# Kernel tuning notes

Measured on AMD Instinct MI355X. Metric: run time of the kernel, lower is better.

The kernel has to match this reference:

```python
import jax, jax.numpy as jnp
import numpy as np

GRID = (32, 512, 512)  # volumetric query grid

def _fade(t):
    # quintic fade: 6t^5 - 15t^4 + 10t^3
    return t * t * t * (t * (t * 6.0 - 15.0) + 10.0)

def _lerp(a, b, t):
    return a + t * (b - a)

def _hash(perm, *indices):
    # chained permutation-table lookup: r = perm[(r + idx) % 256]
    r = jnp.zeros_like(indices[0])
    for idx in indices:
        r = perm[(r + idx) % 256]
    return r

def setup_inputs() -> dict:
    key = jax.random.key(0)
    kx, ky, kz = jax.random.split(key, 3)
    # coordinates uniform in [0, 64) so many lattice cells are covered
    x = jax.random.uniform(kx, GRID, dtype=jnp.float32) * 64.0
    y = jax.random.uniform(ky, GRID, dtype=jnp.float32) * 64.0
    z = jax.random.uniform(kz, GRID, dtype=jnp.float32) * 64.0
    rng = np.random.default_rng(0)
    perm = jnp.asarray(rng.permutation(256), dtype=jnp.int32)
    grad3 = jnp.asarray([
        [1, 1, 0], [-1, 1, 0], [1, -1, 0], [-1, -1, 0],
        [1, 0, 1], [-1, 0, 1], [1, 0, -1], [-1, 0, -1],
        [0, 1, 1], [0, -1, 1], [0, 1, -1], [0, -1, -1]], dtype=jnp.float32)
    return {"x": x, "y": y, "z": z, "perm": perm, "grad3": grad3}

def reference(x, y, z, perm, grad3):
    fx, fy, fz = jnp.floor(x), jnp.floor(y), jnp.floor(z)
    xi = fx.astype(jnp.int32) & 255
    yi = fy.astype(jnp.int32) & 255
    zi = fz.astype(jnp.int32) & 255
    xf, yf, zf = x - fx, y - fy, z - fz
    u, v, w = _fade(xf), _fade(yf), _fade(zf)

    aaa = _hash(perm, xi, yi, zi) % 12
    aab = _hash(perm, xi, yi, zi + 1) % 12
    aba = _hash(perm, xi, yi + 1, zi) % 12
    abb = _hash(perm, xi, yi + 1, zi + 1) % 12
    baa = _hash(perm, xi + 1, yi, zi) % 12
    bab = _hash(perm, xi + 1, yi, zi + 1) % 12
    bba = _hash(perm, xi + 1, yi + 1, zi) % 12
    bbb = _hash(perm, xi + 1, yi + 1, zi + 1) % 12

    def dot3(gi, dx, dy, dz):
        g = grad3[gi]  # gather [..., 3]
        return g[..., 0] * dx + g[..., 1] * dy + g[..., 2] * dz

    g_aaa = dot3(aaa, xf, yf, zf)
    g_aab = dot3(aab, xf, yf, zf - 1)
    g_aba = dot3(aba, xf, yf - 1, zf)
    g_abb = dot3(abb, xf, yf - 1, zf - 1)
    g_baa = dot3(baa, xf - 1, yf, zf)
    g_bab = dot3(bab, xf - 1, yf, zf - 1)
    g_bba = dot3(bba, xf - 1, yf - 1, zf)
    g_bbb = dot3(bbb, xf - 1, yf - 1, zf - 1)

    x1 = _lerp(g_aaa, g_baa, u)
    x2 = _lerp(g_aba, g_bba, u)
    x3 = _lerp(g_aab, g_bab, u)
    x4 = _lerp(g_abb, g_bbb, u)
    y1 = _lerp(x1, x2, v)
    y2 = _lerp(x3, x4, v)
    return _lerp(y1, y2, w)
```

## Files before the change

### kernel.cpp

```cpp
#include <hip/hip_runtime.h>

__global__ __launch_bounds__(256) void perlin_cells(
    const int* __restrict__ perm, unsigned* __restrict__ cellTab)
{
    __shared__ unsigned P[256];
    P[threadIdx.x] = (unsigned)perm[threadIdx.x];
    __syncthreads();

    unsigned id = blockIdx.x * 256 + threadIdx.x;
    unsigned cx = id & 63u, cy = (id >> 6) & 63u, cz = id >> 12;

    unsigned A = P[cx], B = P[cx + 1];
    unsigned t2[2][2];
    t2[0][0] = P[(A + cy) & 255u];
    t2[0][1] = P[(A + cy + 1u) & 255u];
    t2[1][0] = P[(B + cy) & 255u];
    t2[1][1] = P[(B + cy + 1u) & 255u];

    unsigned word = 0;
    #pragma unroll
    for (unsigned bx = 0; bx < 2; ++bx)
      #pragma unroll
      for (unsigned by = 0; by < 2; ++by)
        #pragma unroll
        for (unsigned bz = 0; bz < 2; ++bz) {
            unsigned gi  = P[(t2[bx][by] + cz + bz) & 255u] % 12u;
            unsigned nib = ((unsigned)(gi < 8u) << 3) | ((unsigned)(gi < 4u) << 2)
                         | ((gi & 1u) << 1) | ((gi >> 1) & 1u);
            unsigned e   = (bx << 2) | (by << 1) | bz;
            word |= nib << (4u * e);
        }
    cellTab[id] = word;
}

#define TPB 256
#define NBLOCKS 2048

__device__ __forceinline__ float fade_f(float t) {
    return t * t * t * fmaf(t, fmaf(t, 6.0f, -15.0f), 10.0f);
}
__device__ __forceinline__ float lerp_f(float a, float b, float t) {
    return fmaf(t, b - a, a);
}

__device__ __forceinline__ float gdot_t(unsigned t, float dx, float dy, float dz) {
    float c1 = ((int)t < 0) ? dx : dy;
    float c2 = ((int)(t << 1) < 0) ? dy : dz;
    unsigned r1 = __float_as_uint(c1) ^ ((t << 2) & 0x80000000u);
    unsigned r2 = __float_as_uint(c2) ^ ((t << 3) & 0x80000000u);
    return __uint_as_float(r1) + __uint_as_float(r2);
}

__global__ __launch_bounds__(TPB, 8) void perlin_kernel(
    const float* __restrict__ xg, const float* __restrict__ yg,
    const float* __restrict__ zg, const unsigned* __restrict__ cellTab,
    float* __restrict__ out, int nquads)
{
    const float4* x4 = (const float4*)xg;
    const float4* y4 = (const float4*)yg;
    const float4* z4 = (const float4*)zg;
    float4* o4 = (float4*)out;

    const int stride = gridDim.x * TPB;
    for (int q = blockIdx.x * TPB + threadIdx.x; q < nquads; q += stride) {
        float4 xv = x4[q], yv = y4[q], zv = z4[q];
        float xs[4] = {xv.x, xv.y, xv.z, xv.w};
        float ys[4] = {yv.x, yv.y, yv.z, yv.w};
        float zs[4] = {zv.x, zv.y, zv.z, zv.w};

        int ix[4], iy[4], iz[4];
        unsigned cw[4];
        #pragma unroll
        for (int e = 0; e < 4; ++e) {
            ix[e] = (int)xs[e]; iy[e] = (int)ys[e]; iz[e] = (int)zs[e];
            cw[e] = cellTab[ix[e] + (iy[e] << 6) + (iz[e] << 12)];
        }

        float4 res;
        float* rp = &res.x;
        #pragma unroll
        for (int e = 0; e < 4; ++e) {
            float xf = xs[e] - (float)ix[e];
            float yf = ys[e] - (float)iy[e];
            float zf = zs[e] - (float)iz[e];
            float u = fade_f(xf), v = fade_f(yf), w = fade_f(zf);
            float xf1 = xf - 1.0f, yf1 = yf - 1.0f, zf1 = zf - 1.0f;
            unsigned cwe = cw[e];

            float g_aaa = gdot_t(cwe << 28, xf,  yf,  zf);
            float g_aab = gdot_t(cwe << 24, xf,  yf,  zf1);
            float g_aba = gdot_t(cwe << 20, xf,  yf1, zf);
            float g_abb = gdot_t(cwe << 16, xf,  yf1, zf1);
            float g_baa = gdot_t(cwe << 12, xf1, yf,  zf);
            float g_bab = gdot_t(cwe << 8,  xf1, yf,  zf1);
            float g_bba = gdot_t(cwe << 4,  xf1, yf1, zf);
            float g_bbb = gdot_t(cwe,       xf1, yf1, zf1);

            float l1 = lerp_f(g_aaa, g_baa, u);
            float l2 = lerp_f(g_aba, g_bba, u);
            float l3 = lerp_f(g_aab, g_bab, u);
            float l4 = lerp_f(g_abb, g_bbb, u);
            float m1 = lerp_f(l1, l2, v);
            float m2 = lerp_f(l3, l4, v);
            rp[e] = lerp_f(m1, m2, w);
        }
        o4[q] = res;
    }
}

extern "C" void kernel_launch(void* const* d_in, const int* in_sizes, int n_in,
                              void* d_out, int out_size, void* d_ws, size_t ws_size,
                              hipStream_t stream) {
    const float* x   = (const float*)d_in[0];
    const float* y   = (const float*)d_in[1];
    const float* z   = (const float*)d_in[2];
    const int* perm  = (const int*)d_in[3];
    float* out = (float*)d_out;
    unsigned* cellTab = (unsigned*)d_ws;

    perlin_cells<<<1024, 256, 0, stream>>>(perm, cellTab);

    int nquads = out_size >> 2;
    perlin_kernel<<<NBLOCKS, TPB, 0, stream>>>(x, y, z, cellTab, out, nquads);
}
```

Baseline: 171.9 us.

## Replace global per-cell hash table with factored LDS tables and replicated gradient words

The 256K-entry per-cell gradient table, read from global memory with a random gather for every point, is replaced by two small tables. One is a 65x64 table of second-level hash pairs and the other is a 256-entry table of packed gradient nibbles for z and z+1. Both are copied into LDS in every block, and the gradient table is replicated 16 ways to reduce bank conflicts. Each point now does two LDS loads plus four replicated LDS lookups instead of one global gather. This adds per-block LDS setup (about 33KB), a single-block table-building kernel, and a change to 512 threads per block, which may limit occupancy.

```diff
diff --git a/kernel.cpp b/kernel.cpp
--- a/kernel.cpp
+++ b/kernel.cpp
@@ -1,40 +1,34 @@
 #include <hip/hip_runtime.h>
 
-__global__ __launch_bounds__(256) void perlin_cells(
-    const int* __restrict__ perm, unsigned* __restrict__ cellTab)
+__global__ __launch_bounds__(512) void perlin_tables(
+    const int* __restrict__ perm, unsigned* __restrict__ H2Pg,
+    unsigned* __restrict__ Wg)
 {
     __shared__ unsigned P[256];
-    P[threadIdx.x] = (unsigned)perm[threadIdx.x];
+    if (threadIdx.x < 256) P[threadIdx.x] = (unsigned)perm[threadIdx.x];
     __syncthreads();
-
-    unsigned id = blockIdx.x * 256 + threadIdx.x;
-    unsigned cx = id & 63u, cy = (id >> 6) & 63u, cz = id >> 12;
-
-    unsigned A = P[cx], B = P[cx + 1];
-    unsigned t2[2][2];
-    t2[0][0] = P[(A + cy) & 255u];
-    t2[0][1] = P[(A + cy + 1u) & 255u];
-    t2[1][0] = P[(B + cy) & 255u];
-    t2[1][1] = P[(B + cy + 1u) & 255u];
-
-    unsigned word = 0;
-    #pragma unroll
-    for (unsigned bx = 0; bx < 2; ++bx)
-      #pragma unroll
-      for (unsigned by = 0; by < 2; ++by)
-        #pragma unroll
-        for (unsigned bz = 0; bz < 2; ++bz) {
-            unsigned gi  = P[(t2[bx][by] + cz + bz) & 255u] % 12u;
-            unsigned nib = ((unsigned)(gi < 8u) << 3) | ((unsigned)(gi < 4u) << 2)
-                         | ((gi & 1u) << 1) | ((gi >> 1) & 1u);
-            unsigned e   = (bx << 2) | (by << 1) | bz;
-            word |= nib << (4u * e);
-        }
-    cellTab[id] = word;
+    for (int s = threadIdx.x; s < 65 * 64; s += 512) {
+        unsigned x = (unsigned)s >> 6, y = (unsigned)s & 63u;
+        unsigned b = P[x];
+        unsigned lo = P[(b + y) & 255u] << 6;
+        unsigned hi = P[(b + y + 1u) & 255u] << 6;
+        H2Pg[s] = lo | (hi << 16);
+    }
+    for (int s = threadIdx.x; s < 256; s += 512) {
+        unsigned g0 = P[s] % 12u;
+        unsigned g1 = P[(s + 1u) & 255u] % 12u;
+        unsigned n0 = ((unsigned)(g0 < 8u) << 3) | ((unsigned)(g0 < 4u) << 2)
+                    | ((g0 & 1u) << 1) | ((g0 >> 1) & 1u);
+        unsigned n1 = ((unsigned)(g1 < 8u) << 3) | ((unsigned)(g1 < 4u) << 2)
+                    | ((g1 & 1u) << 1) | ((g1 >> 1) & 1u);
+        Wg[s] = (n0 << 28) | (n1 << 24);
+    }
 }
 
-#define TPB 256
-#define NBLOCKS 2048
+#define TPB 512
+#define NBLOCKS 1024
+#define H2W (65 * 64)
+#define WREPL 16
 
 __device__ __forceinline__ float fade_f(float t) {
     return t * t * t * fmaf(t, fmaf(t, 6.0f, -15.0f), 10.0f);
@@ -42,7 +36,6 @@
 __device__ __forceinline__ float lerp_f(float a, float b, float t) {
     return fmaf(t, b - a, a);
 }
-
 __device__ __forceinline__ float gdot_t(unsigned t, float dx, float dy, float dz) {
     float c1 = ((int)t < 0) ? dx : dy;
     float c2 = ((int)(t << 1) < 0) ? dy : dz;
@@ -53,9 +46,19 @@
 
 __global__ __launch_bounds__(TPB, 8) void perlin_kernel(
     const float* __restrict__ xg, const float* __restrict__ yg,
-    const float* __restrict__ zg, const unsigned* __restrict__ cellTab,
-    float* __restrict__ out, int nquads)
+    const float* __restrict__ zg, const unsigned* __restrict__ H2Pg,
+    const unsigned* __restrict__ Wg, float* __restrict__ out, int nquads)
 {
+    __shared__ unsigned H2[H2W];
+    __shared__ unsigned Wr[256 * WREPL];
+    for (int s = threadIdx.x; s < H2W; s += TPB)         H2[s] = H2Pg[s];
+    for (int s = threadIdx.x; s < 256 * WREPL; s += TPB) Wr[s] = Wg[s >> 4];
+    __syncthreads();
+
+    const unsigned c4 = (threadIdx.x & (WREPL - 1)) << 2;
+    const char* H2b = (const char*)H2;
+    const char* Wb  = (const char*)Wr;
+
     const float4* x4 = (const float4*)xg;
     const float4* y4 = (const float4*)yg;
     const float4* z4 = (const float4*)zg;
@@ -64,46 +67,52 @@
     const int stride = gridDim.x * TPB;
     for (int q = blockIdx.x * TPB + threadIdx.x; q < nquads; q += stride) {
         float4 xv = x4[q], yv = y4[q], zv = z4[q];
-        float xs[4] = {xv.x, xv.y, xv.z, xv.w};
-        float ys[4] = {yv.x, yv.y, yv.z, yv.w};
-        float zs[4] = {zv.x, zv.y, zv.z, zv.w};
+        float4 res;
 
-        int ix[4], iy[4], iz[4];
-        unsigned cw[4];
-        #pragma unroll
-        for (int e = 0; e < 4; ++e) {
-            ix[e] = (int)xs[e]; iy[e] = (int)ys[e]; iz[e] = (int)zs[e];
-            cw[e] = cellTab[ix[e] + (iy[e] << 6) + (iz[e] << 12)];
+        #define CORE(X, Y, Z, OUT) {                                          \
+            int ix = (int)(X), iy = (int)(Y), iz = (int)(Z);                  \
+            float xf = (X) - (float)ix, yf = (Y) - (float)iy,                 \
+                  zf = (Z) - (float)iz;                                       \
+                         \
+            const unsigned* hp =                                              \
+                (const unsigned*)(H2b + ((unsigned)((ix << 6) + iy) << 2));   \
+            unsigned h_a = hp[0], h_b = hp[64];              \
+            unsigned z6 = (unsigned)iz << 6;                                  \
+            \
+            \
+            unsigned ta0 = (h_a + z6) & 0x3FC0u;                              \
+            unsigned ta1 = ((h_a >> 16) + z6) & 0x3FC0u;                      \
+            unsigned tb0 = (h_b + z6) & 0x3FC0u;                              \
+            unsigned tb1 = ((h_b >> 16) + z6) & 0x3FC0u;                      \
+            unsigned w_aa = *(const unsigned*)(Wb + (ta0 | c4));              \
+            unsigned w_ab = *(const unsigned*)(Wb + (ta1 | c4));              \
+            unsigned w_ba = *(const unsigned*)(Wb + (tb0 | c4));              \
+            unsigned w_bb = *(const unsigned*)(Wb + (tb1 | c4));              \
+            float u = fade_f(xf), v = fade_f(yf), w = fade_f(zf);             \
+            float xf1 = xf - 1.0f, yf1 = yf - 1.0f, zf1 = zf - 1.0f;          \
+            float g_aaa = gdot_t(w_aa,      xf,  yf,  zf);                    \
+            float g_aab = gdot_t(w_aa << 4, xf,  yf,  zf1);                   \
+            float g_aba = gdot_t(w_ab,      xf,  yf1, zf);                    \
+            float g_abb = gdot_t(w_ab << 4, xf,  yf1, zf1);                   \
+            float g_baa = gdot_t(w_ba,      xf1, yf,  zf);                    \
+            float g_bab = gdot_t(w_ba << 4, xf1, yf,  zf1);                   \
+            float g_bba = gdot_t(w_bb,      xf1, yf1, zf);                    \
+            float g_bbb = gdot_t(w_bb << 4, xf1, yf1, zf1);                   \
+            float l1 = lerp_f(g_aaa, g_baa, u);                               \
+            float l2 = lerp_f(g_aba, g_bba, u);                               \
+            float l3 = lerp_f(g_aab, g_bab, u);                               \
+            float l4 = lerp_f(g_abb, g_bbb, u);                               \
+            float m1 = lerp_f(l1, l2, v);                                     \
+            float m2 = lerp_f(l3, l4, v);                                     \
+            OUT = lerp_f(m1, m2, w);                                          \
         }
 
-        float4 res;
-        float* rp = &res.x;
-        #pragma unroll
-        for (int e = 0; e < 4; ++e) {
-            float xf = xs[e] - (float)ix[e];
-            float yf = ys[e] - (float)iy[e];
-            float zf = zs[e] - (float)iz[e];
-            float u = fade_f(xf), v = fade_f(yf), w = fade_f(zf);
-            float xf1 = xf - 1.0f, yf1 = yf - 1.0f, zf1 = zf - 1.0f;
-            unsigned cwe = cw[e];
+        CORE(xv.x, yv.x, zv.x, res.x)
+        CORE(xv.y, yv.y, zv.y, res.y)
+        CORE(xv.z, yv.z, zv.z, res.z)
+        CORE(xv.w, yv.w, zv.w, res.w)
+        #undef CORE
 
-            float g_aaa = gdot_t(cwe << 28, xf,  yf,  zf);
-            float g_aab = gdot_t(cwe << 24, xf,  yf,  zf1);
-            float g_aba = gdot_t(cwe << 20, xf,  yf1, zf);
-            float g_abb = gdot_t(cwe << 16, xf,  yf1, zf1);
-            float g_baa = gdot_t(cwe << 12, xf1, yf,  zf);
-            float g_bab = gdot_t(cwe << 8,  xf1, yf,  zf1);
-            float g_bba = gdot_t(cwe << 4,  xf1, yf1, zf);
-            float g_bbb = gdot_t(cwe,       xf1, yf1, zf1);
-
-            float l1 = lerp_f(g_aaa, g_baa, u);
-            float l2 = lerp_f(g_aba, g_bba, u);
-            float l3 = lerp_f(g_aab, g_bab, u);
-            float l4 = lerp_f(g_abb, g_bbb, u);
-            float m1 = lerp_f(l1, l2, v);
-            float m2 = lerp_f(l3, l4, v);
-            rp[e] = lerp_f(m1, m2, w);
-        }
         o4[q] = res;
     }
 }
@@ -111,15 +120,17 @@
 extern "C" void kernel_launch(void* const* d_in, const int* in_sizes, int n_in,
                               void* d_out, int out_size, void* d_ws, size_t ws_size,
                               hipStream_t stream) {
-    const float* x   = (const float*)d_in[0];
-    const float* y   = (const float*)d_in[1];
-    const float* z   = (const float*)d_in[2];
-    const int* perm  = (const int*)d_in[3];
+    const float* x  = (const float*)d_in[0];
+    const float* y  = (const float*)d_in[1];
+    const float* z  = (const float*)d_in[2];
+    const int* perm = (const int*)d_in[3];
     float* out = (float*)d_out;
-    unsigned* cellTab = (unsigned*)d_ws;
 
-    perlin_cells<<<1024, 256, 0, stream>>>(perm, cellTab);
+    unsigned* H2Pg = (unsigned*)d_ws;
+    unsigned* Wg   = H2Pg + H2W;
+
+    perlin_tables<<<1, 512, 0, stream>>>(perm, H2Pg, Wg);
 
     int nquads = out_size >> 2;
-    perlin_kernel<<<NBLOCKS, TPB, 0, stream>>>(x, y, z, cellTab, out, nquads);
+    perlin_kernel<<<NBLOCKS, TPB, 0, stream>>>(x, y, z, H2Pg, Wg, out, nquads);
 }
```

After: 143.8 us. -16.3%, faster.
